# Optimization experiments

Measured on AMD Instinct MI355X. Metric: run time of the kernel, lower is better.

## Reference

```python
import jax, jax.numpy as jnp
import numpy as np

N0, N1, N2 = 320000, 80000, 16000
E1, E2 = 800000, 160000
IN_C, HID, OUT_C = 128, 64, 48
H1, H2 = 4, 1
NEG_SLOPE = 0.2  # PyG GATv2Conv default leaky_relu slope


def _glorot(key, shape):
    fan_in = shape[0]
    return jax.random.normal(key, shape, jnp.float32) / jnp.sqrt(jnp.asarray(fan_in, jnp.float32))


def setup_inputs() -> dict:
    key = jax.random.key(0)
    ks = jax.random.split(key, 12)
    inp = {
        "x": jax.random.normal(ks[0], (N0, IN_C), jnp.float32),
        # layer 1: GATv2Conv(IN_C -> HID, heads=H1, concat=True)
        "Wl1": _glorot(ks[1], (IN_C, H1 * HID)),
        "bl1": jnp.zeros((H1 * HID,), jnp.float32),
        "Wr1": _glorot(ks[2], (IN_C, H1 * HID)),
        "br1": jnp.zeros((H1 * HID,), jnp.float32),
        "att1": jax.random.normal(ks[3], (H1, HID), jnp.float32) * 0.1,
        "bias1": jnp.zeros((H1 * HID,), jnp.float32),
        # layer 2: GATv2Conv(H1*HID -> OUT_C, heads=H2, concat=False)
        "Wl2": _glorot(ks[4], (H1 * HID, H2 * OUT_C)),
        "bl2": jnp.zeros((H2 * OUT_C,), jnp.float32),
        "Wr2": _glorot(ks[5], (H1 * HID, H2 * OUT_C)),
        "br2": jnp.zeros((H2 * OUT_C,), jnp.float32),
        "att2": jax.random.normal(ks[6], (H2, OUT_C), jnp.float32) * 0.1,
        "bias2": jnp.zeros((OUT_C,), jnp.float32),
        # sampled bipartite edge lists (edge j->i: src index into x_src, dst into x_dst)
        "src1": jax.random.randint(ks[7], (E1,), 0, N0, jnp.int32),
        "dst1": jax.random.randint(ks[8], (E1,), 0, N1, jnp.int32),
        "src2": jax.random.randint(ks[9], (E2,), 0, N1, jnp.int32),
        "dst2": jax.random.randint(ks[10], (E2,), 0, N2, jnp.int32),
        "n1": N1,
        "n2": N2,
    }
    return inp


def gatv2_conv(x_src, x_dst, src, dst, Wl, bl, Wr, br, att, bias, n_dst, concat):
    H, C = att.shape
    xl = (x_src @ Wl + bl).reshape(-1, H, C)   # [N_src, H, C] (source transform)
    xr = (x_dst @ Wr + br).reshape(-1, H, C)   # [N_dst, H, C] (target transform)
    e = xl[src] + xr[dst]                      # [E, H, C]
    e = jnp.where(e > 0, e, NEG_SLOPE * e)     # leaky_relu (GATv2: nonlinearity before att)
    alpha = jnp.einsum('ehc,hc->eh', e, att)   # [E, H] attention logits
    # softmax over edges sharing the same target node
    amax = jax.ops.segment_max(alpha, dst, num_segments=n_dst)
    ex = jnp.exp(alpha - amax[dst])
    denom = jax.ops.segment_sum(ex, dst, num_segments=n_dst)
    w = ex / (denom[dst] + 1e-16)              # [E, H]
    out = jax.ops.segment_sum(xl[src] * w[:, :, None], dst, num_segments=n_dst)  # [N_dst, H, C]
    out = out.reshape(n_dst, H * C) if concat else out.mean(axis=1)
    return out + bias


def reference(x, Wl1, bl1, Wr1, br1, att1, bias1, Wl2, bl2, Wr2, br2, att2, bias2,
              src1, dst1, src2, dst2, n1, n2):
    h = gatv2_conv(x, x[:n1], src1, dst1, Wl1, bl1, Wr1, br1, att1, bias1, n1, True)
    h = jax.nn.relu(h)
    # dropout is identity in eval mode
    h = gatv2_conv(h, h[:n2], src2, dst2, Wl2, bl2, Wr2, br2, att2, bias2, n2, False)
    return jax.nn.log_softmax(h, axis=-1)
```

## Files before the change

kernel.cpp:

```cpp
#include <hip/hip_runtime.h>
#include <hip/hip_bf16.h>

#define N0_  320000
#define N1_  80000
#define N2_  16000
#define INC_ 128
#define HID_ 64
#define H1_  4
#define C1_  256
#define OUT_ 48
#define OUTP_ 64
#define NEG_ 0.2f

typedef __attribute__((ext_vector_type(8))) short bfrag8;
typedef __attribute__((ext_vector_type(4))) float ffrag4;

__device__ __forceinline__ float bf2f(unsigned short u){
  unsigned int v = ((unsigned int)u) << 16;
  return __uint_as_float(v);
}
__device__ __forceinline__ unsigned short f2bf(float f){
  unsigned int u = __float_as_uint(f);
  u += 0x7FFFu + ((u >> 16) & 1u);
  return (unsigned short)(u >> 16);
}
__device__ __forceinline__ void unpack2(unsigned int u, float& lo, float& hi){
  lo = __uint_as_float(u << 16);
  hi = __uint_as_float(u & 0xffff0000u);
}

__global__ void transpose_all(const float* __restrict__ Wl1, const float* __restrict__ Wr1,
                              const float* __restrict__ Wl2, const float* __restrict__ Wr2,
                              unsigned short* __restrict__ Wt1l, unsigned short* __restrict__ Wt1r,
                              unsigned short* __restrict__ Wt2l, unsigned short* __restrict__ Wt2r){
  int idx = blockIdx.x*256 + threadIdx.x;
  if (idx < 32768){ int n = idx >> 7, k = idx & 127; Wt1l[idx] = f2bf(Wl1[k*C1_ + n]); }
  else if (idx < 65536){ int j = idx - 32768; int n = j >> 7, k = j & 127; Wt1r[j] = f2bf(Wr1[k*C1_ + n]); }
  else if (idx < 77824){ int j = idx - 65536; int n = j >> 8, k = j & 255; Wt2l[j] = f2bf(Wl2[k*OUT_ + n]); }
  else if (idx < 90112){ int j = idx - 77824; int n = j >> 8, k = j & 255; Wt2r[j] = f2bf(Wr2[k*OUT_ + n]); }
}

__global__ __launch_bounds__(256, 3) void gemm1_fused(
    const float* __restrict__ X,
    const unsigned short* __restrict__ Wtl, const unsigned short* __restrict__ Wtr,
    const float* __restrict__ bl, const float* __restrict__ br,
    unsigned short* __restrict__ outl, unsigned short* __restrict__ outr)
{
  __shared__ unsigned short As[64][136];
  __shared__ unsigned short Cs[64][264];
  const int t = threadIdx.x;
  const int lane = t & 63, wave = t >> 6;
  const int row0 = blockIdx.x << 6;
  const int l15 = lane & 15, q = lane >> 4;
  const int wcol = wave << 6;
  const int c4 = t & 31;

  #pragma unroll
  for (int i = 0; i < 8; ++i){
    int r = (i<<3) + (t>>5);
    float4 xv = *(const float4*)(X + ((size_t)(row0 + r) << 7) + (c4<<2));
    ushort4 s; s.x=f2bf(xv.x); s.y=f2bf(xv.y); s.z=f2bf(xv.z); s.w=f2bf(xv.w);
    *(ushort4*)(&As[r][c4<<2]) = s;
  }
  __syncthreads();

  const int npass = (row0 < N1_) ? 2 : 1;
  for (int pass = 0; pass < npass; ++pass){
    const unsigned short* Wt = pass ? Wtr : Wtl;
    const float* bias = pass ? br : bl;
    unsigned short* out = pass ? outr : outl;

    bfrag8 bfr[4][4];
    #pragma unroll
    for (int nt = 0; nt < 4; ++nt)
      #pragma unroll
      for (int ks = 0; ks < 4; ++ks)
        bfr[nt][ks] = *(const bfrag8*)(Wt + (size_t)(wcol + (nt<<4) + l15)*128 + (ks<<5) + (q<<3));

    ffrag4 z = {0.f, 0.f, 0.f, 0.f};
    ffrag4 acc[4][4];
    #pragma unroll
    for (int mt = 0; mt < 4; ++mt)
      #pragma unroll
      for (int nt = 0; nt < 4; ++nt) acc[mt][nt] = z;

    #pragma unroll
    for (int mt = 0; mt < 4; ++mt){
      #pragma unroll
      for (int ks = 0; ks < 4; ++ks){
        bfrag8 af = *(const bfrag8*)(&As[(mt<<4) + l15][(ks<<5) + (q<<3)]);
        #pragma unroll
        for (int nt = 0; nt < 4; ++nt)
          acc[mt][nt] = __builtin_amdgcn_mfma_f32_16x16x32_bf16(af, bfr[nt][ks], acc[mt][nt], 0, 0, 0);
      }
    }

    float bb[4];
    #pragma unroll
    for (int nt = 0; nt < 4; ++nt) bb[nt] = bias[wcol + (nt<<4) + l15];
    #pragma unroll
    for (int mt = 0; mt < 4; ++mt)
      #pragma unroll
      for (int nt = 0; nt < 4; ++nt)
        #pragma unroll
        for (int rg = 0; rg < 4; ++rg)
          Cs[(mt<<4) + (q<<2) + rg][wcol + (nt<<4) + l15] = f2bf(acc[mt][nt][rg] + bb[nt]);
    __syncthreads();
    #pragma unroll
    for (int i = 0; i < 8; ++i){
      int r = (i<<3) + (t>>5);
      *(bfrag8*)(out + ((size_t)(row0 + r) << 8) + (c4<<3)) = *(const bfrag8*)(&Cs[r][c4<<3]);
    }
    if (pass + 1 < npass) __syncthreads();
  }
}

__global__ __launch_bounds__(256) void gemm2_fused(
    const unsigned short* __restrict__ Hin,
    const unsigned short* __restrict__ Wtl, const unsigned short* __restrict__ Wtr,
    const float* __restrict__ bl, const float* __restrict__ br,
    float* __restrict__ outl, float* __restrict__ outr)
{
  __shared__ unsigned short As2[64][264];
  __shared__ unsigned short Bs2[48][264];
  const int t = threadIdx.x;
  const int lane = t & 63, wave = t >> 6;
  const int row0 = blockIdx.x << 6;
  const int l15 = lane & 15, q = lane >> 4;
  const int c32 = t & 31;

  #pragma unroll
  for (int i = 0; i < 8; ++i){
    int r = (i<<3) + (t>>5);
    *(bfrag8*)(&As2[r][c32<<3]) = *(const bfrag8*)(Hin + ((size_t)(row0 + r) << 8) + (c32<<3));
  }

  const int npass = (row0 < N2_) ? 2 : 1;
  for (int pass = 0; pass < npass; ++pass){
    const unsigned short* Wt = pass ? Wtr : Wtl;
    const float* bias = pass ? br : bl;
    float* out = pass ? outr : outl;

    if (pass) __syncthreads();
    #pragma unroll
    for (int i = 0; i < 6; ++i){
      int idx = i*256 + t;
      int r = idx >> 5, c = (idx & 31) << 3;
      *(bfrag8*)(&Bs2[r][c]) = *(const bfrag8*)(Wt + (size_t)r*256 + c);
    }
    __syncthreads();

    ffrag4 z = {0.f, 0.f, 0.f, 0.f};
    ffrag4 acc[3] = {z, z, z};
    #pragma unroll
    for (int ks = 0; ks < 8; ++ks){
      bfrag8 af = *(const bfrag8*)(&As2[(wave<<4) + l15][(ks<<5) + (q<<3)]);
      #pragma unroll
      for (int nt = 0; nt < 3; ++nt){
        bfrag8 bf = *(const bfrag8*)(&Bs2[(nt<<4) + l15][(ks<<5) + (q<<3)]);
        acc[nt] = __builtin_amdgcn_mfma_f32_16x16x32_bf16(af, bf, acc[nt], 0, 0, 0);
      }
    }
    #pragma unroll
    for (int nt = 0; nt < 3; ++nt){
      int col = (nt<<4) + l15;
      float bb = bias[col];
      #pragma unroll
      for (int rg = 0; rg < 4; ++rg){
        int row = row0 + (wave<<4) + (q<<2) + rg;
        out[(size_t)row*OUTP_ + col] = acc[nt][rg] + bb;
      }
    }
    #pragma unroll
    for (int rg = 0; rg < 4; ++rg){
      int row = row0 + (wave<<4) + (q<<2) + rg;
      out[(size_t)row*OUTP_ + 48 + l15] = 0.f;
    }
  }
}

__global__ void hist_both(const int* __restrict__ dst1, const int* __restrict__ dst2,
                          int* __restrict__ cnt1, int* __restrict__ cnt2, int E1, int E2){
  int i = blockIdx.x*256 + threadIdx.x;
  if (i < E1) atomicAdd(&cnt1[dst1[i]], 1);
  else if (i < E1 + E2) atomicAdd(&cnt2[dst2[i - E1]], 1);
}

__global__ __launch_bounds__(256) void scan_local_both(
    const int* __restrict__ in1, const int* __restrict__ in2,
    int* __restrict__ ex1, int* __restrict__ ex2,
    int* __restrict__ part1, int* __restrict__ part2, int n1, int n2, int nb1){
  __shared__ int s[256];
  const int* in; int* excl; int* partials; int n; int b;
  if ((int)blockIdx.x < nb1){ in = in1; excl = ex1; partials = part1; n = n1; b = blockIdx.x; }
  else { in = in2; excl = ex2; partials = part2; n = n2; b = blockIdx.x - nb1; }
  int t = threadIdx.x, i = b*256 + t;
  int v = (i < n) ? in[i] : 0;
  s[t] = v; __syncthreads();
  #pragma unroll
  for (int off = 1; off < 256; off <<= 1){
    int u = (t >= off) ? s[t-off] : 0;
    __syncthreads();
    s[t] += u; __syncthreads();
  }
  if (i < n) excl[i] = s[t] - v;
  if (t == 255) partials[b] = s[255];
}

__global__ __launch_bounds__(512) void scan_partials_both(
    int* __restrict__ part1, int* __restrict__ part2, int nb1, int nb2){
  __shared__ int s[512];
  int* partials = blockIdx.x ? part2 : part1;
  int nb = blockIdx.x ? nb2 : nb1;
  int t = threadIdx.x;
  int v = (t < nb) ? partials[t] : 0;
  s[t] = v; __syncthreads();
  #pragma unroll
  for (int off = 1; off < 512; off <<= 1){
    int u = (t >= off) ? s[t-off] : 0;
    __syncthreads();
    s[t] += u; __syncthreads();
  }
  if (t < nb) partials[t] = s[t] - v;
}

__global__ void scan_finalize_both(
    int* __restrict__ ex1, int* __restrict__ ex2,
    const int* __restrict__ part1, const int* __restrict__ part2,
    int* __restrict__ cur1, int* __restrict__ cur2, int n1, int n2, int nb1){
  int* excl; const int* partials; int* cursor; int n; int b;
  if ((int)blockIdx.x < nb1){ excl = ex1; partials = part1; cursor = cur1; n = n1; b = blockIdx.x; }
  else { excl = ex2; partials = part2; cursor = cur2; n = n2; b = blockIdx.x - nb1; }
  int i = b*256 + threadIdx.x;
  if (i >= n) return;
  int o = excl[i] + partials[b];
  excl[i] = o; cursor[i] = o;
}

__global__ void scatter_both(const int* __restrict__ src1, const int* __restrict__ dst1,
                             const int* __restrict__ src2, const int* __restrict__ dst2,
                             int* __restrict__ cur1, int* __restrict__ cur2,
                             int* __restrict__ perm1, int* __restrict__ perm2, int E1, int E2){
  int i = blockIdx.x*256 + threadIdx.x;
  if (i < E1){
    int pos = atomicAdd(&cur1[dst1[i]], 1);
    perm1[pos] = src1[i];
  } else if (i < E1 + E2){
    int j = i - E1;
    int pos = atomicAdd(&cur2[dst2[j]], 1);
    perm2[pos] = src2[j];
  }
}

__global__ __launch_bounds__(256) void gat_aggregate1(
    const unsigned short* __restrict__ xl, const unsigned short* __restrict__ xr,
    const int* __restrict__ offsets, const int* __restrict__ counts,
    const int* __restrict__ perm, const float* __restrict__ att,
    const float* __restrict__ bias, unsigned short* __restrict__ hout, int n)
{
  int node = (blockIdx.x << 2) + (threadIdx.x >> 6);
  if (node >= n) return;
  const int lane = threadIdx.x & 63;
  const int slot = lane >> 5;
  const int sub  = lane & 31;
  const int elem = sub << 3;
  const unsigned int ebyte = (unsigned)elem << 1;
  const char* xlb = (const char*)xl;

  const int st = offsets[node], cnt = counts[node];
  uint4 ru = *(const uint4*)(xr + ((size_t)node << 8) + elem);
  float r[8];
  unpack2(ru.x, r[0], r[1]); unpack2(ru.y, r[2], r[3]);
  unpack2(ru.z, r[4], r[5]); unpack2(ru.w, r[6], r[7]);
  float4 al = *(const float4*)(att + elem);
  float4 ah = *(const float4*)(att + elem + 4);
  float a[8] = {al.x, al.y, al.z, al.w, ah.x, ah.y, ah.z, ah.w};

  float acc[8] = {0,0,0,0,0,0,0,0};
  float den = 0.f;

  for (int jb = 0; jb < cnt; jb += 64){
    int m = cnt - jb; if (m > 64) m = 64;
    int pv = (lane < m) ? perm[st + jb + lane] : 0;
    int s_cur = __shfl(pv, slot);
    uint4 xc = *(const uint4*)(xlb + (((unsigned)s_cur << 9) + ebyte));
    for (int j = 0; j < m; j += 2){
      int s_next = __shfl(pv, (j + 2 + slot) & 63);
      uint4 xn = *(const uint4*)(xlb + (((unsigned)s_next << 9) + ebyte));
      float x[8];
      unpack2(xc.x, x[0], x[1]); unpack2(xc.y, x[2], x[3]);
      unpack2(xc.z, x[4], x[5]); unpack2(xc.w, x[6], x[7]);
      float p = 0.f;
      #pragma unroll
      for (int i = 0; i < 8; ++i){
        float v = x[i] + r[i];
        float e = fmaf(NEG_, fminf(v, 0.f), fmaxf(v, 0.f));
        p = fmaf(e, a[i], p);
      }
      p += __shfl_xor(p, 1);
      p += __shfl_xor(p, 2);
      p += __shfl_xor(p, 4);
      float ex = __expf(p);
      ex = (j + slot < m) ? ex : 0.f;
      den += ex;
      #pragma unroll
      for (int i = 0; i < 8; ++i) acc[i] = fmaf(ex, x[i], acc[i]);
      xc = xn;
    }
  }
  den += __shfl_xor(den, 32);
  #pragma unroll
  for (int i = 0; i < 8; ++i) acc[i] += __shfl_xor(acc[i], 32);

  if (slot == 0){
    float w = 1.f / (den + 1e-16f);
    float4 bl = *(const float4*)(bias + elem);
    float4 bh = *(const float4*)(bias + elem + 4);
    float b[8] = {bl.x, bl.y, bl.z, bl.w, bh.x, bh.y, bh.z, bh.w};
    unsigned int o[4];
    #pragma unroll
    for (int i = 0; i < 4; ++i){
      unsigned short lo = f2bf(fmaxf(fmaf(acc[2*i],   w, b[2*i]),   0.f));
      unsigned short hi = f2bf(fmaxf(fmaf(acc[2*i+1], w, b[2*i+1]), 0.f));
      o[i] = (unsigned)lo | ((unsigned)hi << 16);
    }
    *(uint4*)(hout + ((size_t)node << 8) + elem) = make_uint4(o[0], o[1], o[2], o[3]);
  }
}

__global__ __launch_bounds__(256) void gat_aggregate2(
    const float* __restrict__ xl, const float* __restrict__ xr,
    const int* __restrict__ offsets, const int* __restrict__ counts,
    const int* __restrict__ perm, const float* __restrict__ att,
    const float* __restrict__ bias, float* __restrict__ out, int n)
{
  int node = (blockIdx.x << 2) + (threadIdx.x >> 6);
  if (node >= n) return;
  const int lane = threadIdx.x & 63;
  const int slot = lane >> 4;
  const int sub  = lane & 15;
  const bool realc = sub < 12;

  const int st = offsets[node], cnt = counts[node];
  float4 r = *(const float4*)(xr + (size_t)node*OUTP_ + (sub<<2));
  float4 a = realc ? *(const float4*)(att + (sub<<2)) : make_float4(0,0,0,0);
  float4 acc = make_float4(0,0,0,0);
  float den = 0.f;

  for (int jb = 0; jb < cnt; jb += 64){
    int m = cnt - jb; if (m > 64) m = 64;
    int pv = (lane < m) ? perm[st + jb + lane] : 0;
    int s_cur = __shfl(pv, slot);
    float4 xc = *(const float4*)(xl + (size_t)((unsigned)s_cur*OUTP_ + (sub<<2)));
    for (int j = 0; j < m; j += 4){
      int s_next = __shfl(pv, (j + 4 + slot) & 63);
      float4 xn = *(const float4*)(xl + (size_t)((unsigned)s_next*OUTP_ + (sub<<2)));
      float v0 = xc.x + r.x, v1 = xc.y + r.y, v2 = xc.z + r.z, v3 = xc.w + r.w;
      float p;
      p = fmaf(a.x, fmaf(NEG_, fminf(v0,0.f), fmaxf(v0,0.f)), 0.f);
      p = fmaf(a.y, fmaf(NEG_, fminf(v1,0.f), fmaxf(v1,0.f)), p);
      p = fmaf(a.z, fmaf(NEG_, fminf(v2,0.f), fmaxf(v2,0.f)), p);
      p = fmaf(a.w, fmaf(NEG_, fminf(v3,0.f), fmaxf(v3,0.f)), p);
      p += __shfl_xor(p, 1);
      p += __shfl_xor(p, 2);
      p += __shfl_xor(p, 4);
      p += __shfl_xor(p, 8);
      float ex = __expf(p);
      ex = (j + slot < m) ? ex : 0.f;
      den += ex;
      acc.x = fmaf(ex, xc.x, acc.x); acc.y = fmaf(ex, xc.y, acc.y);
      acc.z = fmaf(ex, xc.z, acc.z); acc.w = fmaf(ex, xc.w, acc.w);
      xc = xn;
    }
  }
  den += __shfl_xor(den, 16); den += __shfl_xor(den, 32);
  acc.x += __shfl_xor(acc.x, 16); acc.x += __shfl_xor(acc.x, 32);
  acc.y += __shfl_xor(acc.y, 16); acc.y += __shfl_xor(acc.y, 32);
  acc.z += __shfl_xor(acc.z, 16); acc.z += __shfl_xor(acc.z, 32);
  acc.w += __shfl_xor(acc.w, 16); acc.w += __shfl_xor(acc.w, 32);

  float w = 1.f / (den + 1e-16f);
  float4 b = realc ? *(const float4*)(bias + (sub<<2)) : make_float4(0,0,0,0);
  float v0 = fmaf(acc.x, w, b.x), v1 = fmaf(acc.y, w, b.y);
  float v2 = fmaf(acc.z, w, b.z), v3 = fmaf(acc.w, w, b.w);

  float mx = realc ? fmaxf(fmaxf(v0, v1), fmaxf(v2, v3)) : -3.0e38f;
  mx = fmaxf(mx, __shfl_xor(mx, 1)); mx = fmaxf(mx, __shfl_xor(mx, 2));
  mx = fmaxf(mx, __shfl_xor(mx, 4)); mx = fmaxf(mx, __shfl_xor(mx, 8));
  float es = realc ? (__expf(v0-mx) + __expf(v1-mx) + __expf(v2-mx) + __expf(v3-mx)) : 0.f;
  es += __shfl_xor(es, 1); es += __shfl_xor(es, 2);
  es += __shfl_xor(es, 4); es += __shfl_xor(es, 8);
  float ls = __logf(es);
  if (slot == 0 && realc){
    float4 o = make_float4(v0-mx-ls, v1-mx-ls, v2-mx-ls, v3-mx-ls);
    *(float4*)(out + (size_t)node*OUT_ + (sub<<2)) = o;
  }
}

extern "C" void kernel_launch(void* const* d_in, const int* in_sizes, int n_in,
                              void* d_out, int out_size, void* d_ws, size_t ws_size,
                              hipStream_t stream)
{
  const float* x    = (const float*)d_in[0];
  const float* Wl1  = (const float*)d_in[1];
  const float* bl1  = (const float*)d_in[2];
  const float* Wr1  = (const float*)d_in[3];
  const float* br1  = (const float*)d_in[4];
  const float* att1 = (const float*)d_in[5];
  const float* bias1= (const float*)d_in[6];
  const float* Wl2  = (const float*)d_in[7];
  const float* bl2  = (const float*)d_in[8];
  const float* Wr2  = (const float*)d_in[9];
  const float* br2  = (const float*)d_in[10];
  const float* att2 = (const float*)d_in[11];
  const float* bias2= (const float*)d_in[12];
  const int* src1 = (const int*)d_in[13];
  const int* dst1 = (const int*)d_in[14];
  const int* src2 = (const int*)d_in[15];
  const int* dst2 = (const int*)d_in[16];
  const int E1 = in_sizes[13];
  const int E2 = in_sizes[15];
  (void)n_in; (void)out_size; (void)ws_size;

  char* ws = (char*)d_ws;
  unsigned short* xl1  = (unsigned short*)(ws + 0LL);
  unsigned short* xr1  = (unsigned short*)(ws + 163840000LL);
  unsigned short* hbuf = (unsigned short*)(ws + 204800000LL);
  float* xl2p   = (float*)(ws + 245760000LL);
  float* xr2p   = (float*)(ws + 266240000LL);
  int*   perm1  = (int*)  (ws + 270336000LL);
  int*   perm2  = (int*)  (ws + 273536000LL);
  int*   cnt1   = (int*)  (ws + 274176000LL);
  int*   cnt2   = (int*)  (ws + 274496000LL);
  int*   off1   = (int*)  (ws + 274560000LL);
  int*   cur1   = (int*)  (ws + 274880000LL);
  int*   off2   = (int*)  (ws + 275200000LL);
  int*   cur2   = (int*)  (ws + 275264000LL);
  int*   part1  = (int*)  (ws + 275328000LL);
  int*   part2  = (int*)  (ws + 275330048LL);
  unsigned short* Wt1l = (unsigned short*)(ws + 275332096LL);
  unsigned short* Wt1r = (unsigned short*)(ws + 275397632LL);
  unsigned short* Wt2l = (unsigned short*)(ws + 275463168LL);
  unsigned short* Wt2r = (unsigned short*)(ws + 275487744LL);

  hipMemsetAsync(ws + 274176000LL, 0, 384000LL, stream);

  const int nb1 = (N1_ + 255) / 256;
  const int nb2 = (N2_ + 255) / 256;

  transpose_all<<<352, 256, 0, stream>>>(Wl1, Wr1, Wl2, Wr2, Wt1l, Wt1r, Wt2l, Wt2r);

  hist_both         <<<(E1+E2+255)/256, 256, 0, stream>>>(dst1, dst2, cnt1, cnt2, E1, E2);
  scan_local_both   <<<nb1+nb2, 256, 0, stream>>>(cnt1, cnt2, off1, off2, part1, part2, N1_, N2_, nb1);
  scan_partials_both<<<2, 512, 0, stream>>>(part1, part2, nb1, nb2);
  scan_finalize_both<<<nb1+nb2, 256, 0, stream>>>(off1, off2, part1, part2, cur1, cur2, N1_, N2_, nb1);
  scatter_both      <<<(E1+E2+255)/256, 256, 0, stream>>>(src1, dst1, src2, dst2,
                                                          cur1, cur2, perm1, perm2, E1, E2);

  gemm1_fused<<<N0_/64, 256, 0, stream>>>(x, Wt1l, Wt1r, bl1, br1, xl1, xr1);

  gat_aggregate1<<<(N1_+3)/4, 256, 0, stream>>>(xl1, xr1, off1, cnt1, perm1,
                                                att1, bias1, hbuf, N1_);

  gemm2_fused<<<N1_/64, 256, 0, stream>>>(hbuf, Wt2l, Wt2r, bl2, br2, xl2p, xr2p);

  gat_aggregate2<<<(N2_+3)/4, 256, 0, stream>>>(xl2p, xr2p, off2, cnt2, perm2,
                                                att2, bias2, (float*)d_out, N2_);
}
```

Baseline: 535.2 us.

## Split fused two-pass GEMMs into per-block left/right tiles and cut shared memory

Both projection GEMMs now launch separate blocks for the source (Wl) and target (Wr) transforms instead of having some blocks do two passes, which balances work across blocks. gemm1 reuses a single smaller shared buffer for the A tile and for a half-height output staging area, allowing 4 blocks per CU, and loads B fragments per k-step to lower register pressure. gemm2 drops the shared B tile, holds the weight fragments in registers in three waves, and uses the fourth wave to zero the padding columns. The cost is that the X rows for the first N1 nodes are loaded and converted twice, and the output is staged in two halves with extra barriers.

```diff
diff --git a/kernel.cpp b/kernel.cpp
--- a/kernel.cpp
+++ b/kernel.cpp
@@ -40,17 +40,20 @@
   else if (idx < 90112){ int j = idx - 77824; int n = j >> 8, k = j & 255; Wt2r[j] = f2bf(Wr2[k*OUT_ + n]); }
 }
 
-__global__ __launch_bounds__(256, 3) void gemm1_fused(
+__global__ __launch_bounds__(256, 4) void gemm1_split(
     const float* __restrict__ X,
     const unsigned short* __restrict__ Wtl, const unsigned short* __restrict__ Wtr,
     const float* __restrict__ bl, const float* __restrict__ br,
-    unsigned short* __restrict__ outl, unsigned short* __restrict__ outr)
+    unsigned short* __restrict__ outl, unsigned short* __restrict__ outr, int nblk_l)
 {
-  __shared__ unsigned short As[64][136];
-  __shared__ unsigned short Cs[64][264];
+  __shared__ unsigned short Buf[8704];
   const int t = threadIdx.x;
   const int lane = t & 63, wave = t >> 6;
-  const int row0 = blockIdx.x << 6;
+  const bool isR = (int)blockIdx.x >= nblk_l;
+  const int row0 = (isR ? (int)blockIdx.x - nblk_l : (int)blockIdx.x) << 6;
+  const unsigned short* Wt = isR ? Wtr : Wtl;
+  const float* bias = isR ? br : bl;
+  unsigned short* out = isR ? outr : outl;
   const int l15 = lane & 15, q = lane >> 4;
   const int wcol = wave << 6;
   const int c4 = t & 31;
@@ -60,120 +63,110 @@
     int r = (i<<3) + (t>>5);
     float4 xv = *(const float4*)(X + ((size_t)(row0 + r) << 7) + (c4<<2));
     ushort4 s; s.x=f2bf(xv.x); s.y=f2bf(xv.y); s.z=f2bf(xv.z); s.w=f2bf(xv.w);
-    *(ushort4*)(&As[r][c4<<2]) = s;
+    *(ushort4*)(&Buf[r*136 + (c4<<2)]) = s;
   }
   __syncthreads();
 
-  const int npass = (row0 < N1_) ? 2 : 1;
-  for (int pass = 0; pass < npass; ++pass){
-    const unsigned short* Wt = pass ? Wtr : Wtl;
-    const float* bias = pass ? br : bl;
-    unsigned short* out = pass ? outr : outl;
-
-    bfrag8 bfr[4][4];
+  ffrag4 z = {0.f, 0.f, 0.f, 0.f};
+  ffrag4 acc[4][4];
+  #pragma unroll
+  for (int mt = 0; mt < 4; ++mt)
+    #pragma unroll
+    for (int nt = 0; nt < 4; ++nt) acc[mt][nt] = z;
+
+  #pragma unroll
+  for (int ks = 0; ks < 4; ++ks){
+    bfrag8 bfr[4];
     #pragma unroll
     for (int nt = 0; nt < 4; ++nt)
-      #pragma unroll
-      for (int ks = 0; ks < 4; ++ks)
-        bfr[nt][ks] = *(const bfrag8*)(Wt + (size_t)(wcol + (nt<<4) + l15)*128 + (ks<<5) + (q<<3));
-
-    ffrag4 z = {0.f, 0.f, 0.f, 0.f};
-    ffrag4 acc[4][4];
-    #pragma unroll
-    for (int mt = 0; mt < 4; ++mt)
-      #pragma unroll
-      for (int nt = 0; nt < 4; ++nt) acc[mt][nt] = z;
-
+      bfr[nt] = *(const bfrag8*)(Wt + (size_t)(wcol + (nt<<4) + l15)*128 + (ks<<5) + (q<<3));
     #pragma unroll
     for (int mt = 0; mt < 4; ++mt){
-      #pragma unroll
-      for (int ks = 0; ks < 4; ++ks){
-        bfrag8 af = *(const bfrag8*)(&As[(mt<<4) + l15][(ks<<5) + (q<<3)]);
-        #pragma unroll
-        for (int nt = 0; nt < 4; ++nt)
-          acc[mt][nt] = __builtin_amdgcn_mfma_f32_16x16x32_bf16(af, bfr[nt][ks], acc[mt][nt], 0, 0, 0);
-      }
-    }
-
-    float bb[4];
-    #pragma unroll
-    for (int nt = 0; nt < 4; ++nt) bb[nt] = bias[wcol + (nt<<4) + l15];
-    #pragma unroll
-    for (int mt = 0; mt < 4; ++mt)
+      bfrag8 af = *(const bfrag8*)(&Buf[((mt<<4) + l15)*136 + (ks<<5) + (q<<3)]);
+      #pragma unroll
+      for (int nt = 0; nt < 4; ++nt)
+        acc[mt][nt] = __builtin_amdgcn_mfma_f32_16x16x32_bf16(af, bfr[nt], acc[mt][nt], 0, 0, 0);
+    }
+  }
+
+  float bb[4];
+  #pragma unroll
+  for (int nt = 0; nt < 4; ++nt) bb[nt] = bias[wcol + (nt<<4) + l15];
+
+  #pragma unroll
+  for (int h = 0; h < 2; ++h){
+    __syncthreads();
+    #pragma unroll
+    for (int mh = 0; mh < 2; ++mh){
+      int mt = (h<<1) + mh;
       #pragma unroll
       for (int nt = 0; nt < 4; ++nt)
         #pragma unroll
         for (int rg = 0; rg < 4; ++rg)
-          Cs[(mt<<4) + (q<<2) + rg][wcol + (nt<<4) + l15] = f2bf(acc[mt][nt][rg] + bb[nt]);
+          Buf[((mh<<4) + (q<<2) + rg)*264 + wcol + (nt<<4) + l15] = f2bf(acc[mt][nt][rg] + bb[nt]);
+    }
     __syncthreads();
     #pragma unroll
-    for (int i = 0; i < 8; ++i){
-      int r = (i<<3) + (t>>5);
-      *(bfrag8*)(out + ((size_t)(row0 + r) << 8) + (c4<<3)) = *(const bfrag8*)(&Cs[r][c4<<3]);
-    }
-    if (pass + 1 < npass) __syncthreads();
-  }
-}
-
-__global__ __launch_bounds__(256) void gemm2_fused(
+    for (int i = 0; i < 4; ++i){
+      int idx = (i<<8) + t;
+      int r = idx >> 5, c = (idx & 31) << 3;
+      *(bfrag8*)(out + ((size_t)(row0 + (h<<5) + r) << 8) + c) = *(const bfrag8*)(&Buf[r*264 + c]);
+    }
+  }
+}
+
+__global__ __launch_bounds__(256, 4) void gemm2_split(
     const unsigned short* __restrict__ Hin,
     const unsigned short* __restrict__ Wtl, const unsigned short* __restrict__ Wtr,
     const float* __restrict__ bl, const float* __restrict__ br,
-    float* __restrict__ outl, float* __restrict__ outr)
+    float* __restrict__ outl, float* __restrict__ outr, int nblk_l)
 {
-  __shared__ unsigned short As2[64][264];
-  __shared__ unsigned short Bs2[48][264];
+  __shared__ unsigned short As2[64*264];
   const int t = threadIdx.x;
   const int lane = t & 63, wave = t >> 6;
-  const int row0 = blockIdx.x << 6;
+  const bool isR = (int)blockIdx.x >= nblk_l;
+  const int row0 = (isR ? (int)blockIdx.x - nblk_l : (int)blockIdx.x) << 6;
+  const unsigned short* Wt = isR ? Wtr : Wtl;
+  const float* bias = isR ? br : bl;
+  float* out = isR ? outr : outl;
   const int l15 = lane & 15, q = lane >> 4;
-  const int c32 = t & 31;
 
   #pragma unroll
   for (int i = 0; i < 8; ++i){
-    int r = (i<<3) + (t>>5);
-    *(bfrag8*)(&As2[r][c32<<3]) = *(const bfrag8*)(Hin + ((size_t)(row0 + r) << 8) + (c32<<3));
-  }
-
-  const int npass = (row0 < N2_) ? 2 : 1;
-  for (int pass = 0; pass < npass; ++pass){
-    const unsigned short* Wt = pass ? Wtr : Wtl;
-    const float* bias = pass ? br : bl;
-    float* out = pass ? outr : outl;
-
-    if (pass) __syncthreads();
-    #pragma unroll
-    for (int i = 0; i < 6; ++i){
-      int idx = i*256 + t;
-      int r = idx >> 5, c = (idx & 31) << 3;
-      *(bfrag8*)(&Bs2[r][c]) = *(const bfrag8*)(Wt + (size_t)r*256 + c);
-    }
-    __syncthreads();
-
+    int idx = (i<<8) + t;
+    int r = idx >> 5, c = (idx & 31) << 3;
+    *(bfrag8*)(&As2[r*264 + c]) = *(const bfrag8*)(Hin + ((size_t)(row0 + r) << 8) + c);
+  }
+  __syncthreads();
+
+  if (wave < 3){
+    bfrag8 bfr[8];
+    #pragma unroll
+    for (int ks = 0; ks < 8; ++ks)
+      bfr[ks] = *(const bfrag8*)(Wt + (size_t)((wave<<4) + l15)*256 + (ks<<5) + (q<<3));
     ffrag4 z = {0.f, 0.f, 0.f, 0.f};
-    ffrag4 acc[3] = {z, z, z};
+    ffrag4 acc[4] = {z, z, z, z};
     #pragma unroll
     for (int ks = 0; ks < 8; ++ks){
-      bfrag8 af = *(const bfrag8*)(&As2[(wave<<4) + l15][(ks<<5) + (q<<3)]);
-      #pragma unroll
-      for (int nt = 0; nt < 3; ++nt){
-        bfrag8 bf = *(const bfrag8*)(&Bs2[(nt<<4) + l15][(ks<<5) + (q<<3)]);
-        acc[nt] = __builtin_amdgcn_mfma_f32_16x16x32_bf16(af, bf, acc[nt], 0, 0, 0);
+      #pragma unroll
+      for (int mt = 0; mt < 4; ++mt){
+        bfrag8 af = *(const bfrag8*)(&As2[((mt<<4) + l15)*264 + (ks<<5) + (q<<3)]);
+        acc[mt] = __builtin_amdgcn_mfma_f32_16x16x32_bf16(af, bfr[ks], acc[mt], 0, 0, 0);
       }
     }
-    #pragma unroll
-    for (int nt = 0; nt < 3; ++nt){
-      int col = (nt<<4) + l15;
-      float bb = bias[col];
+    int col = (wave<<4) + l15;
+    float bb = bias[col];
+    #pragma unroll
+    for (int mt = 0; mt < 4; ++mt)
       #pragma unroll
       for (int rg = 0; rg < 4; ++rg){
-        int row = row0 + (wave<<4) + (q<<2) + rg;
-        out[(size_t)row*OUTP_ + col] = acc[nt][rg] + bb;
+        int row = row0 + (mt<<4) + (q<<2) + rg;
+        out[(size_t)row*OUTP_ + col] = acc[mt][rg] + bb;
       }
-    }
-    #pragma unroll
-    for (int rg = 0; rg < 4; ++rg){
-      int row = row0 + (wave<<4) + (q<<2) + rg;
+  } else {
+    #pragma unroll
+    for (int i = 0; i < 16; ++i){
+      int row = row0 + (i<<2) + q;
       out[(size_t)row*OUTP_ + 48 + l15] = 0.f;
     }
   }
@@ -457,12 +450,12 @@
   scatter_both      <<<(E1+E2+255)/256, 256, 0, stream>>>(src1, dst1, src2, dst2,
                                                           cur1, cur2, perm1, perm2, E1, E2);
 
-  gemm1_fused<<<N0_/64, 256, 0, stream>>>(x, Wt1l, Wt1r, bl1, br1, xl1, xr1);
+  gemm1_split<<<N0_/64 + N1_/64, 256, 0, stream>>>(x, Wt1l, Wt1r, bl1, br1, xl1, xr1, N0_/64);
 
   gat_aggregate1<<<(N1_+3)/4, 256, 0, stream>>>(xl1, xr1, off1, cnt1, perm1,
                                                 att1, bias1, hbuf, N1_);
 
-  gemm2_fused<<<N1_/64, 256, 0, stream>>>(hbuf, Wt2l, Wt2r, bl2, br2, xl2p, xr2p);
+  gemm2_split<<<N1_/64 + N2_/64, 256, 0, stream>>>(hbuf, Wt2l, Wt2r, bl2, br2, xl2p, xr2p, N1_/64);
 
   gat_aggregate2<<<(N2_+3)/4, 256, 0, stream>>>(xl2p, xr2p, off2, cnt2, perm2,
                                                 att2, bias2, (float*)d_out, N2_);
```

Result: no change. 545.6 us (+1.9%).
